# Kernel optimization log

Hardware: AMD Instinct MI355X
Metric: run time of the kernel (lower is better)

## Reference

```python
import jax, jax.numpy as jnp
import numpy as np

N = 8192
NFEAT = 256
NHID = 64


def setup_inputs() -> dict:
    key = jax.random.key(0)
    k1, k2, k3, k4, k5 = jax.random.split(key, 5)
    x = jax.random.normal(k1, (N, NFEAT), dtype=jnp.float32)
    # symmetric-normalized-ish dense adjacency (random sparse-like weights)
    adj = jax.random.uniform(k2, (N, N), dtype=jnp.float32)
    W1 = jax.random.normal(k3, (NFEAT, NHID), dtype=jnp.float32) * (1.0 / np.sqrt(NFEAT))
    W2 = jax.random.normal(k4, (NHID, NHID), dtype=jnp.float32) * (1.0 / np.sqrt(NHID))
    W3 = jax.random.normal(k5, (NHID, NHID), dtype=jnp.float32) * (1.0 / np.sqrt(NHID))
    return {"x": x, "adj": adj, "W1": W1, "W2": W2, "W3": W3}


def _gcn(x, adj, W):
    # eval mode: dropout is identity. support = x @ W ; out = adj @ support
    return adj @ (x @ W)


def reference(x, adj, W1, W2, W3):
    h1 = jax.nn.relu(_gcn(x, adj, W1))         # [N, nhid]
    mu = _gcn(h1, adj, W2)                      # [N, nhid]
    logvar = _gcn(h1, adj, W3)                  # [N, nhid]
    z = mu                                      # eval: reparameterize returns mu
    recon = z @ z.T                             # [N, N] inner-product decode, act=identity
    return recon, mu, logvar
```

## Files before the change

kernel.cpp:

```cpp
#include <hip/hip_runtime.h>

typedef __bf16 bf16;
typedef __attribute__((ext_vector_type(4))) __bf16 bf16x4;
typedef __attribute__((ext_vector_type(8))) __bf16 bf16x8;
typedef __attribute__((ext_vector_type(4))) float f32x4;

#define MFMA16(a, b, c) __builtin_amdgcn_mfma_f32_16x16x32_bf16((a), (b), (c), 0, 0, 0)

constexpr int N   = 8192;
constexpr int HID = 64;

template <int EPI>
__global__ __launch_bounds__(256) void gcn_pass(const float* __restrict__ A, int K,
                                                const bf16* __restrict__ Bt,
                                                bf16* __restrict__ outT,
                                                const bf16* __restrict__ W23T,
                                                float* __restrict__ mu,
                                                float* __restrict__ lv) {
  __shared__ bf16  As[4][2][16 * 64];
  __shared__ float Hred[4][16][68];
  __shared__ float Ht[16][72];
  const int tid = threadIdx.x, lane = tid & 63, w = tid >> 6;
  const int r = lane & 15, hi = lane >> 4;
  const int i0 = blockIdx.x * 16;
  const int Kw = K >> 2;
  const int kb0 = w * Kw;
  const int nt = Kw / 64;
  const int aR = hi;
  const int aC = r * 4;

  float4 ra[4][4];
  bf16x8 rb[4][8];
  f32x4 acc[4] = {};

  auto loadA = [&](float4 (&dst)[4], int t) {
    const int k0 = kb0 + t * 64;
#pragma unroll
    for (int s = 0; s < 4; ++s)
      dst[s] = *reinterpret_cast<const float4*>(&A[(size_t)(i0 + 4 * s + aR) * K + k0 + aC]);
  };
  auto loadB = [&](bf16x8 (&dst)[8], int t) {
    const int k0 = kb0 + t * 64;
#pragma unroll
    for (int n = 0; n < 4; ++n)
#pragma unroll
      for (int kk = 0; kk < 2; ++kk)
        dst[n * 2 + kk] = *reinterpret_cast<const bf16x8*>(
            &Bt[(size_t)(n * 16 + r) * K + k0 + kk * 32 + hi * 8]);
  };
  auto writeA = [&](int buf, const float4 (&src)[4]) {
    char* base = (char*)&As[w][buf][0];
#pragma unroll
    for (int s = 0; s < 4; ++s) {
      const int R = 4 * s + aR;
      bf16x4 o;
      o[0] = (bf16)src[s].x; o[1] = (bf16)src[s].y;
      o[2] = (bf16)src[s].z; o[3] = (bf16)src[s].w;
      *reinterpret_cast<bf16x4*>(base + R * 128 + ((aC * 2) ^ ((R & 7) << 4))) = o;
    }
  };
  auto compute = [&](int buf, const bf16x8 (&rbv)[8]) {
    const char* base = (const char*)&As[w][buf][0];
#pragma unroll
    for (int kk = 0; kk < 2; ++kk) {
      const bf16x8 fa = *reinterpret_cast<const bf16x8*>(
          base + r * 128 + ((kk * 64 + hi * 16) ^ ((r & 7) << 4)));
#pragma unroll
      for (int n = 0; n < 4; ++n)
        acc[n] = MFMA16(fa, rbv[n * 2 + kk], acc[n]);
    }
  };

  loadA(ra[0], 0);
  if (nt > 1) loadA(ra[1], 1);
  if (nt > 2) loadA(ra[2], 2);
  if (nt > 3) loadA(ra[3], 3);
  loadB(rb[0], 0);
  if (nt > 1) loadB(rb[1], 1);
  if (nt > 2) loadB(rb[2], 2);
  writeA(0, ra[0]);

  for (int tb = 0; tb < nt; tb += 4) {
#pragma unroll
    for (int u = 0; u < 4; ++u) {
      const int t = tb + u;
      if (t >= nt) continue;
      if (t + 3 < nt) loadB(rb[(u + 3) & 3], t + 3);
      if (t + 4 < nt) loadA(ra[u & 3], t + 4);
      if (t + 1 < nt) writeA((u + 1) & 1, ra[(u + 1) & 3]);
      compute(u & 1, rb[u & 3]);
    }
  }

#pragma unroll
  for (int n = 0; n < 4; ++n)
#pragma unroll
    for (int g = 0; g < 4; ++g)
      Hred[w][hi * 4 + g][n * 16 + r] = acc[n][g];
  __syncthreads();
  {
    const int row = tid >> 4, c4 = (tid & 15) * 4;
    float4 s = {0.f, 0.f, 0.f, 0.f};
#pragma unroll
    for (int q = 0; q < 4; ++q) {
      const float4 v = *reinterpret_cast<const float4*>(&Hred[q][row][c4]);
      s.x += v.x; s.y += v.y; s.z += v.z; s.w += v.w;
    }
    if (EPI == 1) {
      s.x = fmaxf(s.x, 0.f); s.y = fmaxf(s.y, 0.f);
      s.z = fmaxf(s.z, 0.f); s.w = fmaxf(s.w, 0.f);
    }
    *reinterpret_cast<float4*>(&Ht[row][c4]) = s;
  }
  __syncthreads();

  if constexpr (EPI <= 1) {
    const int j = tid >> 2, iq = tid & 3;
    bf16x4 o;
#pragma unroll
    for (int e = 0; e < 4; ++e) o[e] = (bf16)Ht[iq * 4 + e][j];
    *reinterpret_cast<bf16x4*>(&outT[(size_t)j * N + i0 + iq * 4]) = o;
  } else {
    f32x4 a2[2] = {};
#pragma unroll
    for (int kk = 0; kk < 2; ++kk) {
      const float4 t0 = *reinterpret_cast<const float4*>(&Ht[r][kk * 32 + hi * 8]);
      const float4 t1 = *reinterpret_cast<const float4*>(&Ht[r][kk * 32 + hi * 8 + 4]);
      bf16x8 fa;
      fa[0] = (bf16)t0.x; fa[1] = (bf16)t0.y; fa[2] = (bf16)t0.z; fa[3] = (bf16)t0.w;
      fa[4] = (bf16)t1.x; fa[5] = (bf16)t1.y; fa[6] = (bf16)t1.z; fa[7] = (bf16)t1.w;
#pragma unroll
      for (int j = 0; j < 2; ++j) {
        const int q = w * 2 + j;
        const bf16x8 fw = *reinterpret_cast<const bf16x8*>(
            &W23T[(size_t)(q * 16 + r) * 64 + kk * 32 + hi * 8]);
        a2[j] = MFMA16(fa, fw, a2[j]);
      }
    }
#pragma unroll
    for (int j = 0; j < 2; ++j) {
      const int q = w * 2 + j;
      float* dst = (q < 4) ? mu : lv;
      const int cc = (q & 3) * 16 + r;
#pragma unroll
      for (int g = 0; g < 4; ++g)
        dst[(size_t)(i0 + hi * 4 + g) * HID + cc] = a2[j][g];
    }
  }
}

__global__ void prep_weights(const float* __restrict__ W1, const float* __restrict__ W2,
                             const float* __restrict__ W3, bf16* __restrict__ W1T,
                             bf16* __restrict__ W23T) {
  const int idx = blockIdx.x * 256 + threadIdx.x;
  if (idx < 16384) {
    const int j = idx >> 8, k = idx & 255;
    W1T[idx] = (bf16)W1[k * HID + j];
  } else {
    const int g = idx - 16384;
    const int j = g >> 6, c = g & 63;
    W23T[g] = (bf16)(j < 64 ? W2[c * HID + j] : W3[c * HID + (j - 64)]);
  }
}

constexpr int LDT = 72;
__global__ __launch_bounds__(256) void recon_mm(const float* __restrict__ mu,
                                                float* __restrict__ out) {
  __shared__ alignas(16) char pool[128 * LDT * 2 * 2];
  bf16* Am = (bf16*)pool;
  bf16* Bm = (bf16*)(pool + 128 * LDT * 2);
  float* Ct = (float*)pool;
  const int tid = threadIdx.x, lane = tid & 63, wave = tid >> 6;
  const int i0 = blockIdx.x * 128, j0 = blockIdx.y * 128;
  {
    const int rr = tid >> 4, c4 = tid & 15;
#pragma unroll
    for (int s = 0; s < 8; ++s) {
      const int row = rr + s * 16;
      const float4 v = *reinterpret_cast<const float4*>(&mu[(size_t)(i0 + row) * HID + c4 * 4]);
      bf16x4 o;
      o[0] = (bf16)v.x; o[1] = (bf16)v.y; o[2] = (bf16)v.z; o[3] = (bf16)v.w;
      *reinterpret_cast<bf16x4*>(&Am[row * LDT + c4 * 4]) = o;
      const float4 u = *reinterpret_cast<const float4*>(&mu[(size_t)(j0 + row) * HID + c4 * 4]);
      bf16x4 p;
      p[0] = (bf16)u.x; p[1] = (bf16)u.y; p[2] = (bf16)u.z; p[3] = (bf16)u.w;
      *reinterpret_cast<bf16x4*>(&Bm[row * LDT + c4 * 4]) = p;
    }
  }
  __syncthreads();
  f32x4 acc[2][8] = {};
  const int rA = wave * 32 + (lane & 15);
#pragma unroll
  for (int kk = 0; kk < 2; ++kk) {
    const int kb = kk * 32 + ((lane >> 4) << 3);
    const bf16x8 a0 = *reinterpret_cast<const bf16x8*>(&Am[rA * LDT + kb]);
    const bf16x8 a1 = *reinterpret_cast<const bf16x8*>(&Am[(rA + 16) * LDT + kb]);
#pragma unroll
    for (int n = 0; n < 8; ++n) {
      const bf16x8 b = *reinterpret_cast<const bf16x8*>(&Bm[(n * 16 + (lane & 15)) * LDT + kb]);
      acc[0][n] = MFMA16(a0, b, acc[0][n]);
      acc[1][n] = MFMA16(a1, b, acc[1][n]);
    }
  }
  const int r4 = (lane >> 4) << 2, c = lane & 15;
#pragma unroll
  for (int h = 0; h < 2; ++h) {
    __syncthreads();
    if ((wave >> 1) == h) {
      const int rbase = (wave & 1) * 32;
#pragma unroll
      for (int m = 0; m < 2; ++m)
#pragma unroll
        for (int n = 0; n < 8; ++n)
#pragma unroll
          for (int g = 0; g < 4; ++g)
            Ct[(rbase + m * 16 + r4 + g) * 132 + n * 16 + c] = acc[m][n][g];
    }
    __syncthreads();
#pragma unroll
    for (int s = 0; s < 8; ++s) {
      const int idx = tid + s * 256;
      const int row = idx >> 5, q = idx & 31;
      const float4 v = *reinterpret_cast<const float4*>(&Ct[row * 132 + q * 4]);
      *reinterpret_cast<float4*>(&out[(size_t)(i0 + h * 64 + row) * N + j0 + q * 4]) = v;
    }
  }
}

extern "C" void kernel_launch(void* const* d_in, const int* in_sizes, int n_in, void* d_out,
                              int out_size, void* d_ws, size_t ws_size, hipStream_t stream) {
  const float* x   = (const float*)d_in[0];
  const float* adj = (const float*)d_in[1];
  const float* W1  = (const float*)d_in[2];
  const float* W2  = (const float*)d_in[3];
  const float* W3  = (const float*)d_in[4];

  float* out    = (float*)d_out;
  float* recon  = out;
  float* mu_out = out + (size_t)N * N;
  float* lv_out = mu_out + (size_t)N * HID;

  char* scr   = (char*)d_out;
  bf16* S1T   = (bf16*)(scr + 0);
  bf16* h1T   = (bf16*)(scr + (1u << 20));
  bf16* W1T   = (bf16*)(scr + (2u << 20));
  bf16* W23T  = (bf16*)(scr + (2u << 20) + 65536);

  prep_weights<<<96, 256, 0, stream>>>(W1, W2, W3, W1T, W23T);
  gcn_pass<0><<<512, 256, 0, stream>>>(x, 256, W1T, S1T, nullptr, nullptr, nullptr);
  gcn_pass<1><<<512, 256, 0, stream>>>(adj, N, S1T, h1T, nullptr, nullptr, nullptr);
  gcn_pass<2><<<512, 256, 0, stream>>>(adj, N, h1T, nullptr, W23T, mu_out, lv_out);
  recon_mm<<<dim3(64, 64), 256, 0, stream>>>(mu_out, recon);
}
```

Measured before the change: 239.7 us.

## Split adjacency GEMMs along K into two slabs with separate reduce kernels

```diff
diff --git a/kernel.cpp b/kernel.cpp
--- a/kernel.cpp
+++ b/kernel.cpp
@@ -10,24 +10,18 @@
 constexpr int N   = 8192;
 constexpr int HID = 64;
 
-template <int EPI>
-__global__ __launch_bounds__(256) void gcn_pass(const float* __restrict__ A, int K,
-                                                const bf16* __restrict__ Bt,
-                                                bf16* __restrict__ outT,
-                                                const bf16* __restrict__ W23T,
-                                                float* __restrict__ mu,
-                                                float* __restrict__ lv) {
+
+__global__ __launch_bounds__(256) void gcn_pass0(const float* __restrict__ A, int K,
+                                                 const bf16* __restrict__ Bt,
+                                                 bf16* __restrict__ outT) {
   __shared__ bf16  As[4][2][16 * 64];
   __shared__ float Hred[4][16][68];
   __shared__ float Ht[16][72];
   const int tid = threadIdx.x, lane = tid & 63, w = tid >> 6;
   const int r = lane & 15, hi = lane >> 4;
   const int i0 = blockIdx.x * 16;
-  const int Kw = K >> 2;
-  const int kb0 = w * Kw;
-  const int nt = Kw / 64;
-  const int aR = hi;
-  const int aC = r * 4;
+  const int Kw = K >> 2, kb0 = w * Kw, nt = Kw / 64;
+  const int aR = hi, aC = r * 4;
 
   float4 ra[4][4];
   bf16x8 rb[4][8];
@@ -106,61 +100,180 @@
       const float4 v = *reinterpret_cast<const float4*>(&Hred[q][row][c4]);
       s.x += v.x; s.y += v.y; s.z += v.z; s.w += v.w;
     }
-    if (EPI == 1) {
-      s.x = fmaxf(s.x, 0.f); s.y = fmaxf(s.y, 0.f);
-      s.z = fmaxf(s.z, 0.f); s.w = fmaxf(s.w, 0.f);
-    }
     *reinterpret_cast<float4*>(&Ht[row][c4]) = s;
   }
   __syncthreads();
-
-  if constexpr (EPI <= 1) {
-    const int j = tid >> 2, iq = tid & 3;
-    bf16x4 o;
-#pragma unroll
-    for (int e = 0; e < 4; ++e) o[e] = (bf16)Ht[iq * 4 + e][j];
-    *reinterpret_cast<bf16x4*>(&outT[(size_t)j * N + i0 + iq * 4]) = o;
-  } else {
-    f32x4 a2[2] = {};
+  const int j = tid >> 2, iq = tid & 3;
+  bf16x4 o;
+#pragma unroll
+  for (int e = 0; e < 4; ++e) o[e] = (bf16)Ht[iq * 4 + e][j];
+  *reinterpret_cast<bf16x4*>(&outT[(size_t)j * N + i0 + iq * 4]) = o;
+}
+
+__global__ __launch_bounds__(256) void gcn_partial(const float* __restrict__ A, int K,
+                                                   const bf16* __restrict__ Bt,
+                                                   float* __restrict__ pPart) {
+  __shared__ bf16  As[4][2][16 * 64];
+  __shared__ float Hred[4][16][68];
+  __shared__ float Ht[16][72];
+  const int tid = threadIdx.x, lane = tid & 63, w = tid >> 6;
+  const int r = lane & 15, hi = lane >> 4;
+  const int i0 = blockIdx.x * 16;
+  const int Kslab = K / gridDim.y;
+  const int Kw = Kslab >> 2;
+  const int kb0 = blockIdx.y * Kslab + w * Kw;
+  const int nt = Kw / 64;
+  const int aR = hi, aC = r * 4;
+
+  float4 ra[4][4];
+  bf16x8 rb[4][8];
+  f32x4 acc[4] = {};
+
+  auto loadA = [&](float4 (&dst)[4], int t) {
+    const int k0 = kb0 + t * 64;
+#pragma unroll
+    for (int s = 0; s < 4; ++s)
+      dst[s] = *reinterpret_cast<const float4*>(&A[(size_t)(i0 + 4 * s + aR) * K + k0 + aC]);
+  };
+  auto loadB = [&](bf16x8 (&dst)[8], int t) {
+    const int k0 = kb0 + t * 64;
+#pragma unroll
+    for (int n = 0; n < 4; ++n)
+#pragma unroll
+      for (int kk = 0; kk < 2; ++kk)
+        dst[n * 2 + kk] = *reinterpret_cast<const bf16x8*>(
+            &Bt[(size_t)(n * 16 + r) * K + k0 + kk * 32 + hi * 8]);
+  };
+  auto writeA = [&](int buf, const float4 (&src)[4]) {
+    char* base = (char*)&As[w][buf][0];
+#pragma unroll
+    for (int s = 0; s < 4; ++s) {
+      const int R = 4 * s + aR;
+      bf16x4 o;
+      o[0] = (bf16)src[s].x; o[1] = (bf16)src[s].y;
+      o[2] = (bf16)src[s].z; o[3] = (bf16)src[s].w;
+      *reinterpret_cast<bf16x4*>(base + R * 128 + ((aC * 2) ^ ((R & 7) << 4))) = o;
+    }
+  };
+  auto compute = [&](int buf, const bf16x8 (&rbv)[8]) {
+    const char* base = (const char*)&As[w][buf][0];
 #pragma unroll
     for (int kk = 0; kk < 2; ++kk) {
-      const float4 t0 = *reinterpret_cast<const float4*>(&Ht[r][kk * 32 + hi * 8]);
-      const float4 t1 = *reinterpret_cast<const float4*>(&Ht[r][kk * 32 + hi * 8 + 4]);
-      bf16x8 fa;
-      fa[0] = (bf16)t0.x; fa[1] = (bf16)t0.y; fa[2] = (bf16)t0.z; fa[3] = (bf16)t0.w;
-      fa[4] = (bf16)t1.x; fa[5] = (bf16)t1.y; fa[6] = (bf16)t1.z; fa[7] = (bf16)t1.w;
-#pragma unroll
-      for (int j = 0; j < 2; ++j) {
-        const int q = w * 2 + j;
-        const bf16x8 fw = *reinterpret_cast<const bf16x8*>(
-            &W23T[(size_t)(q * 16 + r) * 64 + kk * 32 + hi * 8]);
-        a2[j] = MFMA16(fa, fw, a2[j]);
-      }
-    }
-#pragma unroll
-    for (int j = 0; j < 2; ++j) {
-      const int q = w * 2 + j;
-      float* dst = (q < 4) ? mu : lv;
-      const int cc = (q & 3) * 16 + r;
-#pragma unroll
-      for (int g = 0; g < 4; ++g)
-        dst[(size_t)(i0 + hi * 4 + g) * HID + cc] = a2[j][g];
-    }
-  }
-}
-
-__global__ void prep_weights(const float* __restrict__ W1, const float* __restrict__ W2,
-                             const float* __restrict__ W3, bf16* __restrict__ W1T,
-                             bf16* __restrict__ W23T) {
+      const bf16x8 fa = *reinterpret_cast<const bf16x8*>(
+          base + r * 128 + ((kk * 64 + hi * 16) ^ ((r & 7) << 4)));
+#pragma unroll
+      for (int n = 0; n < 4; ++n)
+        acc[n] = MFMA16(fa, rbv[n * 2 + kk], acc[n]);
+    }
+  };
+
+  loadA(ra[0], 0);
+  loadA(ra[1], 1);
+  loadA(ra[2], 2);
+  loadA(ra[3], 3);
+  loadB(rb[0], 0);
+  loadB(rb[1], 1);
+  loadB(rb[2], 2);
+  writeA(0, ra[0]);
+
+  for (int tb = 0; tb < nt; tb += 4) {
+#pragma unroll
+    for (int u = 0; u < 4; ++u) {
+      const int t = tb + u;
+      if (t + 3 < nt) loadB(rb[(u + 3) & 3], t + 3);
+      if (t + 4 < nt) loadA(ra[u & 3], t + 4);
+      if (t + 1 < nt) writeA((u + 1) & 1, ra[(u + 1) & 3]);
+      compute(u & 1, rb[u & 3]);
+    }
+  }
+
+#pragma unroll
+  for (int n = 0; n < 4; ++n)
+#pragma unroll
+    for (int g = 0; g < 4; ++g)
+      Hred[w][hi * 4 + g][n * 16 + r] = acc[n][g];
+  __syncthreads();
+  {
+    const int row = tid >> 4, c4 = (tid & 15) * 4;
+    float4 s = {0.f, 0.f, 0.f, 0.f};
+#pragma unroll
+    for (int q = 0; q < 4; ++q) {
+      const float4 v = *reinterpret_cast<const float4*>(&Hred[q][row][c4]);
+      s.x += v.x; s.y += v.y; s.z += v.z; s.w += v.w;
+    }
+    float* dst = pPart + (size_t)blockIdx.y * N * HID;
+    *reinterpret_cast<float4*>(&dst[(size_t)(i0 + row) * HID + c4]) = s;
+  }
+}
+
+__global__ __launch_bounds__(256) void reduce_relu_T(const float* __restrict__ pB,
+                                                     bf16* __restrict__ h1T) {
+  __shared__ float t[64][65];
+  const int i0 = blockIdx.x * 64;
+  const int tid = threadIdx.x;
+#pragma unroll
+  for (int s = 0; s < 4; ++s) {
+    const int idx = tid + s * 256;
+    const int row = idx >> 4, c4 = idx & 15;
+    const size_t off = (size_t)(i0 + row) * HID + c4 * 4;
+    const float4 v0 = *reinterpret_cast<const float4*>(&pB[off]);
+    const float4 v1 = *reinterpret_cast<const float4*>(&pB[(size_t)N * HID + off]);
+    t[row][c4 * 4 + 0] = fmaxf(v0.x + v1.x, 0.f);
+    t[row][c4 * 4 + 1] = fmaxf(v0.y + v1.y, 0.f);
+    t[row][c4 * 4 + 2] = fmaxf(v0.z + v1.z, 0.f);
+    t[row][c4 * 4 + 3] = fmaxf(v0.w + v1.w, 0.f);
+  }
+  __syncthreads();
+#pragma unroll
+  for (int s = 0; s < 2; ++s) {
+    const int idx = tid + s * 256;
+    const int j = idx >> 3, q = idx & 7;
+    bf16x8 o;
+#pragma unroll
+    for (int e = 0; e < 8; ++e) o[e] = (bf16)t[q * 8 + e][j];
+    *reinterpret_cast<bf16x8*>(&h1T[(size_t)j * N + i0 + q * 8]) = o;
+  }
+}
+
+__global__ __launch_bounds__(256) void reduce_w23_mulv(const float* __restrict__ pC,
+                                                       const float* __restrict__ W2,
+                                                       const float* __restrict__ W3,
+                                                       float* __restrict__ mu,
+                                                       float* __restrict__ lv) {
+  __shared__ float Hs[64][65];
+  __shared__ float Ws[64][128];
+  const int i0 = blockIdx.x * 64;
+  const int tid = threadIdx.x;
+#pragma unroll
+  for (int s = 0; s < 32; ++s) {
+    const int idx = tid + s * 256;
+    const int c = idx >> 7, j = idx & 127;
+    Ws[c][j] = (j < 64) ? W2[c * HID + j] : W3[c * HID + (j - 64)];
+  }
+#pragma unroll
+  for (int s8 = 0; s8 < 16; ++s8) {
+    const int idx = tid + s8 * 256;
+    const int rr = idx >> 6, c = idx & 63;
+    const size_t off = (size_t)(i0 + rr) * HID + c;
+    Hs[rr][c] = pC[off] + pC[(size_t)N * HID + off];
+  }
+  __syncthreads();
+  const int j = tid & 127, ih = tid >> 7;
+  for (int ii = ih; ii < 64; ii += 2) {
+    float a = 0.0f;
+#pragma unroll
+    for (int c = 0; c < 64; ++c) a += Hs[ii][c] * Ws[c][j];
+    if (j < 64)
+      mu[(size_t)(i0 + ii) * HID + j] = a;
+    else
+      lv[(size_t)(i0 + ii) * HID + (j - 64)] = a;
+  }
+}
+
+__global__ void prep_w1t(const float* __restrict__ W1, bf16* __restrict__ W1T) {
   const int idx = blockIdx.x * 256 + threadIdx.x;
-  if (idx < 16384) {
-    const int j = idx >> 8, k = idx & 255;
-    W1T[idx] = (bf16)W1[k * HID + j];
-  } else {
-    const int g = idx - 16384;
-    const int j = g >> 6, c = g & 63;
-    W23T[g] = (bf16)(j < 64 ? W2[c * HID + j] : W3[c * HID + (j - 64)]);
-  }
+  const int j = idx >> 8, k = idx & 255;
+  W1T[idx] = (bf16)W1[k * HID + j];
 }
 
 constexpr int LDT = 72;
@@ -241,14 +354,17 @@
   float* lv_out = mu_out + (size_t)N * HID;
 
   char* scr   = (char*)d_out;
-  bf16* S1T   = (bf16*)(scr + 0);
-  bf16* h1T   = (bf16*)(scr + (1u << 20));
-  bf16* W1T   = (bf16*)(scr + (2u << 20));
-  bf16* W23T  = (bf16*)(scr + (2u << 20) + 65536);
-
-  prep_weights<<<96, 256, 0, stream>>>(W1, W2, W3, W1T, W23T);
-  gcn_pass<0><<<512, 256, 0, stream>>>(x, 256, W1T, S1T, nullptr, nullptr, nullptr);
-  gcn_pass<1><<<512, 256, 0, stream>>>(adj, N, S1T, h1T, nullptr, nullptr, nullptr);
-  gcn_pass<2><<<512, 256, 0, stream>>>(adj, N, h1T, nullptr, W23T, mu_out, lv_out);
+  bf16*  S1T  = (bf16*)(scr + 0);
+  bf16*  h1T  = (bf16*)(scr + (1u << 20));
+  bf16*  W1T  = (bf16*)(scr + (2u << 20));
+  float* pP1  = (float*)(scr + (3u << 20));
+  float* pP2  = (float*)(scr + (7u << 20));
+
+  prep_w1t<<<64, 256, 0, stream>>>(W1, W1T);
+  gcn_pass0<<<512, 256, 0, stream>>>(x, 256, W1T, S1T);
+  gcn_partial<<<dim3(512, 2), 256, 0, stream>>>(adj, N, S1T, pP1);
+  reduce_relu_T<<<128, 256, 0, stream>>>(pP1, h1T);
+  gcn_partial<<<dim3(512, 2), 256, 0, stream>>>(adj, N, h1T, pP2);
+  reduce_w23_mulv<<<128, 256, 0, stream>>>(pP2, W2, W3, mu_out, lv_out);
   recon_mm<<<dim3(64, 64), 256, 0, stream>>>(mu_out, recon);
 }
```

After: 281.1 us. 1.17x slower.

## Specialize adjacency GEMM kernel with 256-wide coalesced chunk loads and double buffering

Applied to the files above, without the earlier changes.

```diff
diff --git a/kernel.cpp b/kernel.cpp
--- a/kernel.cpp
+++ b/kernel.cpp
@@ -11,23 +11,149 @@
 constexpr int HID = 64;
 
 template <int EPI>
-__global__ __launch_bounds__(256) void gcn_pass(const float* __restrict__ A, int K,
-                                                const bf16* __restrict__ Bt,
-                                                bf16* __restrict__ outT,
-                                                const bf16* __restrict__ W23T,
-                                                float* __restrict__ mu,
-                                                float* __restrict__ lv) {
+__global__ __launch_bounds__(256) void gcn_adj(const float* __restrict__ A,
+                                               const bf16* __restrict__ Bt,
+                                               bf16* __restrict__ outT,
+                                               const bf16* __restrict__ W23T,
+                                               float* __restrict__ mu,
+                                               float* __restrict__ lv) {
+  __shared__ bf16  As[4][16 * 256];
+  __shared__ float Hred[4][16][68];
+  __shared__ float Ht[16][72];
+  const int tid = threadIdx.x, lane = tid & 63, w = tid >> 6;
+  const int r = lane & 15, hi = lane >> 4;
+  const int i0 = blockIdx.x * 16;
+  const int kb0 = w * 2048;
+  constexpr int NSC = 8;
+
+  float4 ra[2][16];
+  bf16x8 rb[2][8];
+  f32x4 acc[4] = {};
+
+  auto loadChunk = [&](float4 (&dst)[16], int c) {
+    const int k0 = kb0 + c * 256;
+#pragma unroll
+    for (int i = 0; i < 16; ++i)
+      dst[i] = *reinterpret_cast<const float4*>(&A[(size_t)(i0 + i) * N + k0 + lane * 4]);
+  };
+  auto loadB = [&](bf16x8 (&dst)[8], int T) {
+    const int k0 = kb0 + T * 64;
+#pragma unroll
+    for (int n = 0; n < 4; ++n)
+#pragma unroll
+      for (int kk = 0; kk < 2; ++kk)
+        dst[n * 2 + kk] = *reinterpret_cast<const bf16x8*>(
+            &Bt[(size_t)(n * 16 + r) * N + k0 + kk * 32 + hi * 8]);
+  };
+  auto writeChunk = [&](const float4 (&src)[16]) {
+    char* base = (char*)&As[w][0];
+    const int cl = lane >> 1, bsub = (lane & 1) * 8;
+#pragma unroll
+    for (int i = 0; i < 16; ++i) {
+      bf16x4 o;
+      o[0] = (bf16)src[i].x; o[1] = (bf16)src[i].y;
+      o[2] = (bf16)src[i].z; o[3] = (bf16)src[i].w;
+      *reinterpret_cast<bf16x4*>(base + i * 512 + (cl ^ (i & 7)) * 16 + bsub) = o;
+    }
+  };
+  auto computeTile = [&](int tt, const bf16x8 (&rbv)[8]) {
+    const char* base = (const char*)&As[w][0];
+#pragma unroll
+    for (int kk = 0; kk < 2; ++kk) {
+      const int phys = (tt * 8 + kk * 4 + hi) ^ (r & 7);
+      const bf16x8 fa = *reinterpret_cast<const bf16x8*>(base + r * 512 + phys * 16);
+#pragma unroll
+      for (int n = 0; n < 4; ++n)
+        acc[n] = MFMA16(fa, rbv[n * 2 + kk], acc[n]);
+    }
+  };
+
+  loadChunk(ra[0], 0);
+  loadChunk(ra[1], 1);
+  loadB(rb[0], 0);
+  loadB(rb[1], 1);
+  writeChunk(ra[0]);
+
+#pragma unroll
+  for (int c = 0; c < NSC; ++c) {
+#pragma unroll
+    for (int tt = 0; tt < 4; ++tt) {
+      const int T = c * 4 + tt;
+      computeTile(tt, rb[T & 1]);
+      if (T + 2 < NSC * 4) loadB(rb[T & 1], T + 2);
+    }
+    if (c + 1 < NSC) writeChunk(ra[(c + 1) & 1]);
+    if (c + 2 < NSC) loadChunk(ra[c & 1], c + 2);
+  }
+
+#pragma unroll
+  for (int n = 0; n < 4; ++n)
+#pragma unroll
+    for (int g = 0; g < 4; ++g)
+      Hred[w][hi * 4 + g][n * 16 + r] = acc[n][g];
+  __syncthreads();
+  {
+    const int row = tid >> 4, c4 = (tid & 15) * 4;
+    float4 s = {0.f, 0.f, 0.f, 0.f};
+#pragma unroll
+    for (int q = 0; q < 4; ++q) {
+      const float4 v = *reinterpret_cast<const float4*>(&Hred[q][row][c4]);
+      s.x += v.x; s.y += v.y; s.z += v.z; s.w += v.w;
+    }
+    if (EPI == 1) {
+      s.x = fmaxf(s.x, 0.f); s.y = fmaxf(s.y, 0.f);
+      s.z = fmaxf(s.z, 0.f); s.w = fmaxf(s.w, 0.f);
+    }
+    *reinterpret_cast<float4*>(&Ht[row][c4]) = s;
+  }
+  __syncthreads();
+
+  if constexpr (EPI == 1) {
+    const int j = tid >> 2, iq = tid & 3;
+    bf16x4 o;
+#pragma unroll
+    for (int e = 0; e < 4; ++e) o[e] = (bf16)Ht[iq * 4 + e][j];
+    *reinterpret_cast<bf16x4*>(&outT[(size_t)j * N + i0 + iq * 4]) = o;
+  } else {
+    f32x4 a2[2] = {};
+#pragma unroll
+    for (int kk = 0; kk < 2; ++kk) {
+      const float4 t0 = *reinterpret_cast<const float4*>(&Ht[r][kk * 32 + hi * 8]);
+      const float4 t1 = *reinterpret_cast<const float4*>(&Ht[r][kk * 32 + hi * 8 + 4]);
+      bf16x8 fa;
+      fa[0] = (bf16)t0.x; fa[1] = (bf16)t0.y; fa[2] = (bf16)t0.z; fa[3] = (bf16)t0.w;
+      fa[4] = (bf16)t1.x; fa[5] = (bf16)t1.y; fa[6] = (bf16)t1.z; fa[7] = (bf16)t1.w;
+#pragma unroll
+      for (int j = 0; j < 2; ++j) {
+        const int q = w * 2 + j;
+        const bf16x8 fw = *reinterpret_cast<const bf16x8*>(
+            &W23T[(size_t)(q * 16 + r) * 64 + kk * 32 + hi * 8]);
+        a2[j] = MFMA16(fa, fw, a2[j]);
+      }
+    }
+#pragma unroll
+    for (int j = 0; j < 2; ++j) {
+      const int q = w * 2 + j;
+      float* dst = (q < 4) ? mu : lv;
+      const int cc = (q & 3) * 16 + r;
+#pragma unroll
+      for (int g = 0; g < 4; ++g)
+        dst[(size_t)(i0 + hi * 4 + g) * HID + cc] = a2[j][g];
+    }
+  }
+}
+
+__global__ __launch_bounds__(256) void gcn_pass0(const float* __restrict__ A, int K,
+                                                 const bf16* __restrict__ Bt,
+                                                 bf16* __restrict__ outT) {
   __shared__ bf16  As[4][2][16 * 64];
   __shared__ float Hred[4][16][68];
   __shared__ float Ht[16][72];
   const int tid = threadIdx.x, lane = tid & 63, w = tid >> 6;
   const int r = lane & 15, hi = lane >> 4;
   const int i0 = blockIdx.x * 16;
-  const int Kw = K >> 2;
-  const int kb0 = w * Kw;
-  const int nt = Kw / 64;
-  const int aR = hi;
-  const int aC = r * 4;
+  const int Kw = K >> 2, kb0 = w * Kw, nt = Kw / 64;
+  const int aR = hi, aC = r * 4;
 
   float4 ra[4][4];
   bf16x8 rb[4][8];
@@ -72,22 +198,18 @@
   };
 
   loadA(ra[0], 0);
-  if (nt > 1) loadA(ra[1], 1);
-  if (nt > 2) loadA(ra[2], 2);
-  if (nt > 3) loadA(ra[3], 3);
   loadB(rb[0], 0);
-  if (nt > 1) loadB(rb[1], 1);
-  if (nt > 2) loadB(rb[2], 2);
   writeA(0, ra[0]);
-
   for (int tb = 0; tb < nt; tb += 4) {
 #pragma unroll
     for (int u = 0; u < 4; ++u) {
       const int t = tb + u;
       if (t >= nt) continue;
-      if (t + 3 < nt) loadB(rb[(u + 3) & 3], t + 3);
-      if (t + 4 < nt) loadA(ra[u & 3], t + 4);
-      if (t + 1 < nt) writeA((u + 1) & 1, ra[(u + 1) & 3]);
+      if (t + 1 < nt) {
+        loadA(ra[(u + 1) & 3], t + 1);
+        loadB(rb[(u + 1) & 3], t + 1);
+        writeA((u + 1) & 1, ra[(u + 1) & 3]);
+      }
       compute(u & 1, rb[u & 3]);
     }
   }
@@ -106,47 +228,14 @@
       const float4 v = *reinterpret_cast<const float4*>(&Hred[q][row][c4]);
       s.x += v.x; s.y += v.y; s.z += v.z; s.w += v.w;
     }
-    if (EPI == 1) {
-      s.x = fmaxf(s.x, 0.f); s.y = fmaxf(s.y, 0.f);
-      s.z = fmaxf(s.z, 0.f); s.w = fmaxf(s.w, 0.f);
-    }
     *reinterpret_cast<float4*>(&Ht[row][c4]) = s;
   }
   __syncthreads();
-
-  if constexpr (EPI <= 1) {
-    const int j = tid >> 2, iq = tid & 3;
-    bf16x4 o;
-#pragma unroll
-    for (int e = 0; e < 4; ++e) o[e] = (bf16)Ht[iq * 4 + e][j];
-    *reinterpret_cast<bf16x4*>(&outT[(size_t)j * N + i0 + iq * 4]) = o;
-  } else {
-    f32x4 a2[2] = {};
-#pragma unroll
-    for (int kk = 0; kk < 2; ++kk) {
-      const float4 t0 = *reinterpret_cast<const float4*>(&Ht[r][kk * 32 + hi * 8]);
-      const float4 t1 = *reinterpret_cast<const float4*>(&Ht[r][kk * 32 + hi * 8 + 4]);
-      bf16x8 fa;
-      fa[0] = (bf16)t0.x; fa[1] = (bf16)t0.y; fa[2] = (bf16)t0.z; fa[3] = (bf16)t0.w;
-      fa[4] = (bf16)t1.x; fa[5] = (bf16)t1.y; fa[6] = (bf16)t1.z; fa[7] = (bf16)t1.w;
-#pragma unroll
-      for (int j = 0; j < 2; ++j) {
-        const int q = w * 2 + j;
-        const bf16x8 fw = *reinterpret_cast<const bf16x8*>(
-            &W23T[(size_t)(q * 16 + r) * 64 + kk * 32 + hi * 8]);
-        a2[j] = MFMA16(fa, fw, a2[j]);
-      }
-    }
-#pragma unroll
-    for (int j = 0; j < 2; ++j) {
-      const int q = w * 2 + j;
-      float* dst = (q < 4) ? mu : lv;
-      const int cc = (q & 3) * 16 + r;
-#pragma unroll
-      for (int g = 0; g < 4; ++g)
-        dst[(size_t)(i0 + hi * 4 + g) * HID + cc] = a2[j][g];
-    }
-  }
+  const int j = tid >> 2, iq = tid & 3;
+  bf16x4 o;
+#pragma unroll
+  for (int e = 0; e < 4; ++e) o[e] = (bf16)Ht[iq * 4 + e][j];
+  *reinterpret_cast<bf16x4*>(&outT[(size_t)j * N + i0 + iq * 4]) = o;
 }
 
 __global__ void prep_weights(const float* __restrict__ W1, const float* __restrict__ W2,
@@ -247,8 +336,8 @@
   bf16* W23T  = (bf16*)(scr + (2u << 20) + 65536);
 
   prep_weights<<<96, 256, 0, stream>>>(W1, W2, W3, W1T, W23T);
-  gcn_pass<0><<<512, 256, 0, stream>>>(x, 256, W1T, S1T, nullptr, nullptr, nullptr);
-  gcn_pass<1><<<512, 256, 0, stream>>>(adj, N, S1T, h1T, nullptr, nullptr, nullptr);
-  gcn_pass<2><<<512, 256, 0, stream>>>(adj, N, h1T, nullptr, W23T, mu_out, lv_out);
+  gcn_pass0<<<512, 256, 0, stream>>>(x, 256, W1T, S1T);
+  gcn_adj<1><<<512, 256, 0, stream>>>(adj, S1T, h1T, nullptr, nullptr, nullptr);
+  gcn_adj<2><<<512, 256, 0, stream>>>(adj, h1T, nullptr, W23T, mu_out, lv_out);
   recon_mm<<<dim3(64, 64), 256, 0, stream>>>(mu_out, recon);
 }
```

After: 249.3 us. 1.04x slower.
